# Performance work log

Hardware: AMD Instinct MI355X
Metric: run time of the kernel (lower is better)

## Reference

```python
import jax, jax.numpy as jnp
import numpy as np

ITERS = 2
EPS = 1e-6

_OFFSETS = [(a, b, c) for a in (-1, 0, 1) for b in (-1, 0, 1) for c in (-1, 0, 1)]


def _erosion_step(im):
    # product over full 3x3x3 neighborhood (connectivity=26 -> all 27 voxels),
    # out-of-bounds padded with 1 (identity for product)
    B, C, D, H, W = im.shape
    p = jnp.pad(im, ((0, 0), (0, 0), (1, 1), (1, 1), (1, 1)), constant_values=1.0)
    prod = jnp.ones_like(im)
    for dz, dy, dx in _OFFSETS:
        prod = prod * p[:, :, 1 + dz:1 + dz + D, 1 + dy:1 + dy + H, 1 + dx:1 + dx + W]
    return prod


def _distance_map(im, iters=ITERS):
    # PositiveDistanceMap: dils = -SoftErosion3D(1-im) where SoftErosion3D
    # returns temp = -sum_k im_k (im_0 = 1-im, im_{k+1} = im_k * erosion(im_k))
    cur = 1.0 - im
    acc = jnp.zeros_like(cur)
    for _ in range(iters):
        acc = acc + cur
        cur = cur * _erosion_step(cur)
    return acc


def _lah_loss(x, y_onehot):
    axes = (2, 3, 4)  # batch_lah=False -> per (batch, class) reduction
    dm_hat = _distance_map(x)
    dm_gt = _distance_map(y_onehot)
    fp = (dm_gt * x).sum(axes)
    fn = (dm_hat * y_onehot).sum(axes)
    # norm == 0
    fp = fp / (x.sum(axes) + EPS)
    fn = fn / (y_onehot.sum(axes) + EPS)
    lah = (fp + fn + jnp.abs(fp - fn)) / 2  # logsum2 == elementwise max
    return lah[:, 1:].mean()  # do_bg=False drops background channel


def setup_inputs() -> dict:
    key = jax.random.key(0)
    k1, k2 = jax.random.split(key)
    x = jax.random.uniform(k1, (2, 4, 128, 128, 128), dtype=jnp.float32)
    y = jax.random.randint(k2, (2, 1, 128, 128, 128), 0, 4, dtype=jnp.int64)
    return {"x": x, "y": y}


def reference(x, y):
    C = x.shape[1]
    y_onehot = jax.nn.one_hot(y[:, 0], C, axis=1, dtype=x.dtype)  # [B,C,D,H,W]
    return _lah_loss(x, y_onehot)
```

## Files before the change

### kernel.cpp

```cpp
#include <hip/hip_runtime.h>

constexpr int SPB = 1 << 21;
constexpr float EPSV = 1e-6f;

__device__ unsigned char g_mask[2 * SPB];

constexpr int K0_ZSEG = 4;
constexpr int K0_NBLK = (2 * (128 / K0_ZSEG) * 128) / 4;

struct MEnt { int pk, cx, cy; };

__device__ __forceinline__ MEnt k0_load(const int* __restrict__ yb, int s,
                                        int rbase0, bool ym1, bool yp1) {
    MEnt e;
    const int rb = (s << 14) | rbase0;
    int2 vc = *(const int2*)(yb + rb);
    int nib0 = 1 << vc.x, nib1 = 1 << vc.y;
    if (ym1) { int2 vm = *(const int2*)(yb + rb - 128); nib0 |= 1 << vm.x; nib1 |= 1 << vm.y; }
    if (yp1) { int2 vp = *(const int2*)(yb + rb + 128); nib0 |= 1 << vp.x; nib1 |= 1 << vp.y; }
    e.pk = nib0 | (nib1 << 8);
    e.cx = vc.x; e.cy = vc.y;
    return e;
}

__global__ __launch_bounds__(256) void mask_build(const int* __restrict__ y32) {
    const int wid = (blockIdx.x << 2) | (threadIdx.x >> 6);
    const int lane = threadIdx.x & 63;
    const int yy = wid & 127;
    const int zs = (wid >> 7) & 31;
    const int b = (wid >> 12) & 1;
    const int x0 = lane << 1;
    const int z0 = zs * K0_ZSEG;
    const bool ym1 = yy > 0, yp1 = yy < 127;
    const int rbase0 = (yy << 7) | x0;

    const int* __restrict__ yb = y32 + ((long)b << 21);
    unsigned char* __restrict__ mb = g_mask + ((long)b << 21);

    MEnt e0, e1;
    if (z0 > 0) e0 = k0_load(yb, z0 - 1, rbase0, ym1, yp1);
    else { e0.pk = 0; e0.cx = 0; e0.cy = 0; }
    e1 = k0_load(yb, z0, rbase0, ym1, yp1);

#pragma unroll
    for (int dz = 0; dz < K0_ZSEG; ++dz) {
        const int z = z0 + dz;
        MEnt e2;
        if (z + 1 < 128) e2 = k0_load(yb, z + 1, rbase0, ym1, yp1);
        else { e2.pk = 0; e2.cx = 0; e2.cy = 0; }

        const int zor = e0.pk | e1.pk | e2.pk;
        int orL = __shfl_up(zor, 1);
        if (lane == 0) orL = 0;
        int orR = __shfl_down(zor, 1);
        if (lane == 63) orR = 0;
        const int full0 = (zor | (zor >> 8) | (orL >> 8)) & 15;
        const int full1 = (zor | (zor >> 8) | orR) & 15;

        const unsigned short st =
            (unsigned short)((full0 | (e1.cx << 4)) | ((full1 | (e1.cy << 4)) << 8));
        *(unsigned short*)(mb + ((z << 14) | rbase0)) = st;

        e0 = e1; e1 = e2;
    }
}

constexpr int NBLK = 2048;

__global__ __launch_bounds__(256) void lah_flat(const float* __restrict__ x,
                                                float* __restrict__ acc) {
    __shared__ float sred[4];

    const int bid = blockIdx.x;
    const int plane = bid & 7;
    const int b = plane >> 2, cls = plane & 3;
    const int inner = bid >> 3;
    const int yq = inner & 31;
    const int zc = inner >> 5;
    const int t = threadIdx.x;
    const int w = t >> 6;
    const int lane = t & 63;
    const int y = yq * 4 + w;
    const int z0 = zc * 16;
    const int xo = lane << 1;

    const float* __restrict__ xp = x + ((long)plane << 21);
    const unsigned char* __restrict__ mb = g_mask + ((long)b << 21);

    const bool ym = (y > 0), yp = (y < 127);
    const int base = (y << 7) + xo;

    auto ld = [&](int z, int dy, bool ok) -> float2 {
        if (!ok || (unsigned)z > 127u) return make_float2(0.f, 0.f);
        return *(const float2*)(xp + (z << 14) + base + (dy << 7));
    };

    float fp = 0.f, fn = 0.f, sx = 0.f, sy = 0.f;

#pragma unroll 1
    for (int dz = 0; dz < 16; dz += 2) {
        const int z = z0 + dz;

        float2 r0m = ld(z - 1, -1, ym), r0c = ld(z - 1, 0, true), r0p = ld(z - 1, 1, yp);
        float2 r1m = ld(z,     -1, ym), r1c = ld(z,     0, true), r1p = ld(z,     1, yp);
        float2 r2m = ld(z + 1, -1, ym), r2c = ld(z + 1, 0, true), r2p = ld(z + 1, 1, yp);
        float2 r3m = ld(z + 2, -1, ym), r3c = ld(z + 2, 0, true), r3p = ld(z + 2, 1, yp);
        const unsigned mA = *(const unsigned short*)(mb + (z << 14) + base);
        const unsigned mB = *(const unsigned short*)(mb + ((z + 1) << 14) + base);

        float2 yp0, yp1, yp2, yp3;
        yp0.x = (1.f - r0m.x) * (1.f - r0c.x) * (1.f - r0p.x);
        yp0.y = (1.f - r0m.y) * (1.f - r0c.y) * (1.f - r0p.y);
        yp1.x = (1.f - r1m.x) * (1.f - r1c.x) * (1.f - r1p.x);
        yp1.y = (1.f - r1m.y) * (1.f - r1c.y) * (1.f - r1p.y);
        yp2.x = (1.f - r2m.x) * (1.f - r2c.x) * (1.f - r2p.x);
        yp2.y = (1.f - r2m.y) * (1.f - r2c.y) * (1.f - r2p.y);
        yp3.x = (1.f - r3m.x) * (1.f - r3c.x) * (1.f - r3p.x);
        yp3.y = (1.f - r3m.y) * (1.f - r3c.y) * (1.f - r3p.y);

        const float2 zA = make_float2(yp0.x * yp1.x * yp2.x, yp0.y * yp1.y * yp2.y);
        const float2 zB = make_float2(yp1.x * yp2.x * yp3.x, yp1.y * yp2.y * yp3.y);

        float lA = __shfl_up(zA.y, 1);  if (lane == 0)  lA = 1.f;
        float rA = __shfl_down(zA.x, 1); if (lane == 63) rA = 1.f;
        float lB = __shfl_up(zB.y, 1);  if (lane == 0)  lB = 1.f;
        float rB = __shfl_down(zB.x, 1); if (lane == 63) rB = 1.f;
        const float cA = zA.x * zA.y, cB = zB.x * zB.y;
        const float PA0 = lA * cA, PA1 = cA * rA;
        const float PB0 = lB * cB, PB1 = cB * rB;

        {
            const int m0 = mA & 0xFF, m1 = (mA >> 8) & 0xFF;
            const bool pr0 = (m0 >> cls) & 1, pr1 = (m1 >> cls) & 1;
            const bool eq0 = (m0 >> 4) == cls, eq1 = (m1 >> 4) == cls;
            sx += r1c.x + r1c.y;
            fp += eq0 ? 0.f : r1c.x * (pr0 ? 1.f : 2.f);
            fp += eq1 ? 0.f : r1c.y * (pr1 ? 1.f : 2.f);
            fn += eq0 ? (1.f - r1c.x) * (1.f + PA0) : 0.f;
            fn += eq1 ? (1.f - r1c.y) * (1.f + PA1) : 0.f;
            sy += (eq0 ? 1.f : 0.f) + (eq1 ? 1.f : 0.f);
        }
        {
            const int m0 = mB & 0xFF, m1 = (mB >> 8) & 0xFF;
            const bool pr0 = (m0 >> cls) & 1, pr1 = (m1 >> cls) & 1;
            const bool eq0 = (m0 >> 4) == cls, eq1 = (m1 >> 4) == cls;
            sx += r2c.x + r2c.y;
            fp += eq0 ? 0.f : r2c.x * (pr0 ? 1.f : 2.f);
            fp += eq1 ? 0.f : r2c.y * (pr1 ? 1.f : 2.f);
            fn += eq0 ? (1.f - r2c.x) * (1.f + PB0) : 0.f;
            fn += eq1 ? (1.f - r2c.y) * (1.f + PB1) : 0.f;
            sy += (eq0 ? 1.f : 0.f) + (eq1 ? 1.f : 0.f);
        }
    }

    float rr4[4] = {fp, fn, sx, sy};
#pragma unroll
    for (int i = 0; i < 4; ++i) {
        float vv = rr4[i];
#pragma unroll
        for (int off = 32; off >= 1; off >>= 1) vv += __shfl_down(vv, off);
        rr4[i] = vv;
    }
    if (t < 4) sred[t] = 0.f;
    __syncthreads();
    if (lane == 0) {
#pragma unroll
        for (int i = 0; i < 4; ++i) atomicAdd(&sred[i], rr4[i]);
    }
    __syncthreads();
    if (t < 4)
        atomicAdd(&acc[b * 16 + t * 4 + cls], sred[t]);
}

__global__ void lah_finalize(const float* __restrict__ acc, float* __restrict__ out) {
    float loss = 0.f;
#pragma unroll
    for (int b = 0; b < 2; ++b) {
#pragma unroll
        for (int c = 1; c < 4; ++c) {
            const float fp = acc[b * 16 + 0 + c];
            const float fn = acc[b * 16 + 4 + c];
            const float sxv = acc[b * 16 + 8 + c];
            const float syv = acc[b * 16 + 12 + c];
            loss += fmaxf(fp / (sxv + EPSV), fn / (syv + EPSV));
        }
    }
    out[0] = loss / 6.f;
}

extern "C" void kernel_launch(void* const* d_in, const int* in_sizes, int n_in,
                              void* d_out, int out_size, void* d_ws, size_t ws_size,
                              hipStream_t stream) {
    const float* x = (const float*)d_in[0];
    const int* y32 = (const int*)d_in[1];
    float* out = (float*)d_out;
    float* acc = (float*)d_ws;

    hipMemsetAsync(d_ws, 0, 32 * sizeof(float), stream);
    mask_build<<<K0_NBLK, 256, 0, stream>>>(y32);
    lah_flat<<<NBLK, 256, 0, stream>>>(x, acc);
    lah_finalize<<<1, 1, 0, stream>>>(acc, out);
}
```

Measured before the change: 51.90 us.

## March along y with rolling register window to reuse row loads

Reassigns each wave to a fixed pair of z planes and iterates over 8 consecutive y rows, keeping the three y-rows of four z-slabs in registers and loading only the new leading row per step. This cuts the number of global loads per output from twelve rows per z-pair to four, and precomputes 1-x at load time. It changes the block tiling to 8 y by 8 z, which alters L2 locality and adds register pressure for the window.

After: 65.73 us. +26.6%, slower.

```diff
diff --git a/kernel.cpp b/kernel.cpp
--- a/kernel.cpp
+++ b/kernel.cpp
@@ -67,89 +67,106 @@
 
 constexpr int NBLK = 2048;
 
-__global__ __launch_bounds__(256) void lah_flat(const float* __restrict__ x,
-                                                float* __restrict__ acc) {
+__global__ __launch_bounds__(256) void lah_y(const float* __restrict__ x,
+                                             float* __restrict__ acc) {
     __shared__ float sred[4];
 
     const int bid = blockIdx.x;
     const int plane = bid & 7;
     const int b = plane >> 2, cls = plane & 3;
     const int inner = bid >> 3;
-    const int yq = inner & 31;
-    const int zc = inner >> 5;
+    const int zq = inner & 15;
+    const int yc = inner >> 4;
     const int t = threadIdx.x;
     const int w = t >> 6;
     const int lane = t & 63;
-    const int y = yq * 4 + w;
-    const int z0 = zc * 16;
+    const int zp = zq * 4 + w;
+    const int z0 = zp * 2;
+    const int y0 = yc * 8;
     const int xo = lane << 1;
 
     const float* __restrict__ xp = x + ((long)plane << 21);
     const unsigned char* __restrict__ mb = g_mask + ((long)b << 21);
 
-    const bool ym = (y > 0), yp = (y < 127);
-    const int base = (y << 7) + xo;
-
-    auto ld = [&](int z, int dy, bool ok) -> float2 {
-        if (!ok || (unsigned)z > 127u) return make_float2(0.f, 0.f);
-        return *(const float2*)(xp + (z << 14) + base + (dy << 7));
+    const bool s0ok = (z0 > 0);
+    const bool s3ok = (z0 + 2 < 128);
+
+    auto ldr = [&](int s, int y) -> float2 {
+        const bool ok = (s == 0 ? s0ok : (s == 3 ? s3ok : true)) &&
+                        ((unsigned)y <= 127u);
+        if (!ok) return make_float2(1.f, 1.f);
+        const float2 v = *(const float2*)(xp + ((z0 - 1 + s) << 14) + (y << 7) + xo);
+        return make_float2(1.f - v.x, 1.f - v.y);
     };
 
     float fp = 0.f, fn = 0.f, sx = 0.f, sy = 0.f;
 
-#pragma unroll 1
-    for (int dz = 0; dz < 16; dz += 2) {
-        const int z = z0 + dz;
-
-        float2 r0m = ld(z - 1, -1, ym), r0c = ld(z - 1, 0, true), r0p = ld(z - 1, 1, yp);
-        float2 r1m = ld(z,     -1, ym), r1c = ld(z,     0, true), r1p = ld(z,     1, yp);
-        float2 r2m = ld(z + 1, -1, ym), r2c = ld(z + 1, 0, true), r2p = ld(z + 1, 1, yp);
-        float2 r3m = ld(z + 2, -1, ym), r3c = ld(z + 2, 0, true), r3p = ld(z + 2, 1, yp);
-        const unsigned mA = *(const unsigned short*)(mb + (z << 14) + base);
-        const unsigned mB = *(const unsigned short*)(mb + ((z + 1) << 14) + base);
-
-        float2 yp0, yp1, yp2, yp3;
-        yp0.x = (1.f - r0m.x) * (1.f - r0c.x) * (1.f - r0p.x);
-        yp0.y = (1.f - r0m.y) * (1.f - r0c.y) * (1.f - r0p.y);
-        yp1.x = (1.f - r1m.x) * (1.f - r1c.x) * (1.f - r1p.x);
-        yp1.y = (1.f - r1m.y) * (1.f - r1c.y) * (1.f - r1p.y);
-        yp2.x = (1.f - r2m.x) * (1.f - r2c.x) * (1.f - r2p.x);
-        yp2.y = (1.f - r2m.y) * (1.f - r2c.y) * (1.f - r2p.y);
-        yp3.x = (1.f - r3m.x) * (1.f - r3c.x) * (1.f - r3p.x);
-        yp3.y = (1.f - r3m.y) * (1.f - r3c.y) * (1.f - r3p.y);
-
-        const float2 zA = make_float2(yp0.x * yp1.x * yp2.x, yp0.y * yp1.y * yp2.y);
-        const float2 zB = make_float2(yp1.x * yp2.x * yp3.x, yp1.y * yp2.y * yp3.y);
-
-        float lA = __shfl_up(zA.y, 1);  if (lane == 0)  lA = 1.f;
-        float rA = __shfl_down(zA.x, 1); if (lane == 63) rA = 1.f;
-        float lB = __shfl_up(zB.y, 1);  if (lane == 0)  lB = 1.f;
-        float rB = __shfl_down(zB.x, 1); if (lane == 63) rB = 1.f;
-        const float cA = zA.x * zA.y, cB = zB.x * zB.y;
+    float2 om[4][3];
+#pragma unroll
+    for (int s = 0; s < 4; ++s) {
+        om[s][0] = ldr(s, y0 - 1);
+        om[s][1] = ldr(s, y0);
+    }
+
+#pragma unroll
+    for (int dy = 0; dy < 8; ++dy) {
+        const int y = y0 + dy;
+
+#pragma unroll
+        for (int s = 0; s < 4; ++s) om[s][2] = ldr(s, y + 1);
+        const unsigned mA = *(const unsigned short*)(mb + (z0 << 14) + (y << 7) + xo);
+        const unsigned mB = *(const unsigned short*)(mb + ((z0 + 1) << 14) + (y << 7) + xo);
+
+        float ypx[4], ypy[4];
+#pragma unroll
+        for (int s = 0; s < 4; ++s) {
+            ypx[s] = om[s][0].x * om[s][1].x * om[s][2].x;
+            ypy[s] = om[s][0].y * om[s][1].y * om[s][2].y;
+        }
+
+        const float zAx = ypx[0] * ypx[1] * ypx[2];
+        const float zAy = ypy[0] * ypy[1] * ypy[2];
+        const float zBx = ypx[1] * ypx[2] * ypx[3];
+        const float zBy = ypy[1] * ypy[2] * ypy[3];
+
+        float lA = __shfl_up(zAy, 1);   if (lane == 0)  lA = 1.f;
+        float rA = __shfl_down(zAx, 1); if (lane == 63) rA = 1.f;
+        float lB = __shfl_up(zBy, 1);   if (lane == 0)  lB = 1.f;
+        float rB = __shfl_down(zBx, 1); if (lane == 63) rB = 1.f;
+        const float cA = zAx * zAy, cB = zBx * zBy;
         const float PA0 = lA * cA, PA1 = cA * rA;
         const float PB0 = lB * cB, PB1 = cB * rB;
+
+        const float xA0 = 1.f - om[1][1].x, xA1 = 1.f - om[1][1].y;
+        const float xB0 = 1.f - om[2][1].x, xB1 = 1.f - om[2][1].y;
 
         {
             const int m0 = mA & 0xFF, m1 = (mA >> 8) & 0xFF;
             const bool pr0 = (m0 >> cls) & 1, pr1 = (m1 >> cls) & 1;
             const bool eq0 = (m0 >> 4) == cls, eq1 = (m1 >> 4) == cls;
-            sx += r1c.x + r1c.y;
-            fp += eq0 ? 0.f : r1c.x * (pr0 ? 1.f : 2.f);
-            fp += eq1 ? 0.f : r1c.y * (pr1 ? 1.f : 2.f);
-            fn += eq0 ? (1.f - r1c.x) * (1.f + PA0) : 0.f;
-            fn += eq1 ? (1.f - r1c.y) * (1.f + PA1) : 0.f;
+            sx += xA0 + xA1;
+            fp += eq0 ? 0.f : xA0 * (pr0 ? 1.f : 2.f);
+            fp += eq1 ? 0.f : xA1 * (pr1 ? 1.f : 2.f);
+            fn += eq0 ? om[1][1].x * (1.f + PA0) : 0.f;
+            fn += eq1 ? om[1][1].y * (1.f + PA1) : 0.f;
             sy += (eq0 ? 1.f : 0.f) + (eq1 ? 1.f : 0.f);
         }
         {
             const int m0 = mB & 0xFF, m1 = (mB >> 8) & 0xFF;
             const bool pr0 = (m0 >> cls) & 1, pr1 = (m1 >> cls) & 1;
             const bool eq0 = (m0 >> 4) == cls, eq1 = (m1 >> 4) == cls;
-            sx += r2c.x + r2c.y;
-            fp += eq0 ? 0.f : r2c.x * (pr0 ? 1.f : 2.f);
-            fp += eq1 ? 0.f : r2c.y * (pr1 ? 1.f : 2.f);
-            fn += eq0 ? (1.f - r2c.x) * (1.f + PB0) : 0.f;
-            fn += eq1 ? (1.f - r2c.y) * (1.f + PB1) : 0.f;
+            sx += xB0 + xB1;
+            fp += eq0 ? 0.f : xB0 * (pr0 ? 1.f : 2.f);
+            fp += eq1 ? 0.f : xB1 * (pr1 ? 1.f : 2.f);
+            fn += eq0 ? om[2][1].x * (1.f + PB0) : 0.f;
+            fn += eq1 ? om[2][1].y * (1.f + PB1) : 0.f;
             sy += (eq0 ? 1.f : 0.f) + (eq1 ? 1.f : 0.f);
+        }
+
+#pragma unroll
+        for (int s = 0; s < 4; ++s) {
+            om[s][0] = om[s][1];
+            om[s][1] = om[s][2];
         }
     }
 
@@ -198,6 +215,6 @@
 
     hipMemsetAsync(d_ws, 0, 32 * sizeof(float), stream);
     mask_build<<<K0_NBLK, 256, 0, stream>>>(y32);
-    lah_flat<<<NBLK, 256, 0, stream>>>(x, acc);
+    lah_y<<<NBLK, 256, 0, stream>>>(x, acc);
     lah_finalize<<<1, 1, 0, stream>>>(acc, out);
 }
```
